# Kernel optimization log

Hardware: AMD Instinct MI355X
Metric: run time of the kernel (lower is better)

## Reference

```python
import jax, jax.numpy as jnp
import numpy as np

N_NODES = 50000
N_EDGES = 800000
D_IN = 256
D_OUT = 128


def setup_inputs() -> dict:
    key = jax.random.key(0)
    k1, k2, k3 = jax.random.split(key, 3)
    x = jax.random.normal(k1, (N_NODES, D_IN), dtype=jnp.float32)
    edge_index = jax.random.randint(k2, (2, N_EDGES), 0, N_NODES, dtype=jnp.int64)
    W = jax.random.normal(k3, (D_IN, D_OUT), dtype=jnp.float32) / np.sqrt(D_IN)
    b = jnp.zeros((D_OUT,), dtype=jnp.float32)
    prelu_a = jnp.full((D_OUT,), 0.25, dtype=jnp.float32)  # PyTorch PReLU default init
    return {"x": x, "edge_index": edge_index, "W": W, "b": b, "prelu_a": prelu_a}


def reference(x, edge_index, W, b, prelu_a):
    N = x.shape[0]
    # GCNConv default: add self-loops, symmetric deg^{-1/2} normalization
    self_loops = jnp.arange(N, dtype=edge_index.dtype)
    src = jnp.concatenate([edge_index[0], self_loops])  # message source j
    dst = jnp.concatenate([edge_index[1], self_loops])  # aggregation target i
    deg = jax.ops.segment_sum(jnp.ones_like(dst, dtype=x.dtype), dst, num_segments=N)
    dinv = jnp.where(deg > 0, jax.lax.rsqrt(deg), 0.0)
    norm = dinv[src] * dinv[dst]  # [E+N]
    h = x @ W  # [N, D_OUT] linear transform before aggregation
    msg = h[src] * norm[:, None]  # gather + scale
    out = jax.ops.segment_sum(msg, dst, num_segments=N) + b  # scatter-add + bias
    # per-channel PReLU
    return jnp.where(out > 0, out, prelu_a * out)
```

## Files before the change

### kernel.cpp

```cpp
#include <hip/hip_runtime.h>

#define N_NODES 50000
#define N_EDGES 800000
#define D_IN    256
#define D_OUT   128
#define ELL_S   64
#define GEMM_BLKS ((N_NODES + 127) / 128)
#define BKT_BLKS  ((N_EDGES + 255) / 256)
#define CNT_PAD   50176

typedef __attribute__((ext_vector_type(8))) short short8;
typedef __attribute__((ext_vector_type(4))) float floatx4;

__device__ __forceinline__ unsigned short f2bf(float f) {
    unsigned int u = __float_as_uint(f);
    unsigned int r = (u + 0x7fffu + ((u >> 16) & 1u)) >> 16;
    return (unsigned short)r;
}
__device__ __forceinline__ unsigned int pack2(float a, float b) {
    return (unsigned int)f2bf(a) | ((unsigned int)f2bf(b) << 16);
}
__device__ __forceinline__ float bfl(unsigned int u) { return __uint_as_float(u << 16); }
__device__ __forceinline__ float bfh(unsigned int u) { return __uint_as_float(u & 0xffff0000u); }

__device__ __forceinline__ int load_idx(const void* ei, int i, int is64) {
    if (is64) return (int)((const long long*)ei)[i];
    return ((const int*)ei)[i];
}

__global__ __launch_bounds__(256) void prep_kernel(const unsigned int* __restrict__ e,
                                                   int* __restrict__ is64,
                                                   const float* __restrict__ W,
                                                   unsigned short* __restrict__ bf,
                                                   int* __restrict__ cnt) {
    int bid = blockIdx.x;
    int tid = threadIdx.x;
    if (bid == 0) {
        __shared__ int found32;
        if (tid == 0) found32 = 0;
        __syncthreads();
        for (int i = tid; i < 2048; i += 256)
            if (e[2 * i + 1] != 0u) found32 = 1;
        __syncthreads();
        if (tid == 0) *is64 = (found32 ? 0 : 1);
    } else if (bid <= 16) {
        int g = (bid - 1) * 256 + tid;
        int lane = g & 63;
        int kc   = (g >> 6) & 7;
        int ct   = g >> 9;
        int n  = ct * 16 + (lane & 15);
        int kb = kc * 32 + ((lane >> 4) & 3) * 8;
        unsigned int p[4];
#pragma unroll
        for (int jj = 0; jj < 4; jj++) {
            float a = W[(size_t)(kb + 2 * jj + 0) * D_OUT + n];
            float b = W[(size_t)(kb + 2 * jj + 1) * D_OUT + n];
            p[jj] = pack2(a, b);
        }
        *(uint4*)&bf[(size_t)g * 8] = make_uint4(p[0], p[1], p[2], p[3]);
    } else {
        int i0 = ((bid - 17) * 256 + tid) * 2;
        *(int2*)&cnt[i0] = make_int2(0, 0);
    }
}

__global__ __launch_bounds__(256) void fused_kernel(const float* __restrict__ x,
                                                    const unsigned short* __restrict__ bf,
                                                    unsigned short* __restrict__ h,
                                                    const void* __restrict__ ei,
                                                    const int* __restrict__ is64p,
                                                    int* __restrict__ cnt,
                                                    int* __restrict__ bucket) {
    __shared__ unsigned short As[128][40];
    int tid = threadIdx.x;

    if (blockIdx.x >= GEMM_BLKS) {
        int e = (blockIdx.x - GEMM_BLKS) * 256 + tid;
        if (e < N_EDGES) {
            int is64 = *is64p;
            int s = load_idx(ei, e, is64);
            int d = load_idx(ei, N_EDGES + e, is64);
            int pos = atomicAdd(&cnt[d], 1);
            if (pos < ELL_S) bucket[d * ELL_S + pos] = s;
        }
        return;
    }

    int row0 = blockIdx.x * 128;
    int w    = tid >> 6;
    int lane = tid & 63;
    int quad = lane >> 4;
    int l15  = lane & 15;

    floatx4 acc[2][8];
#pragma unroll
    for (int i = 0; i < 2; i++)
#pragma unroll
        for (int j = 0; j < 8; j++) acc[i][j] = (floatx4){0.f, 0.f, 0.f, 0.f};

    int srow  = tid >> 1;
    int shalf = (tid & 1) * 16;
    const float* xrow = x + (size_t)(row0 + srow) * D_IN;
    bool svalid = (row0 + srow) < N_NODES;

    for (int k0 = 0; k0 < D_IN; k0 += 32) {
        uint4 p0 = make_uint4(0, 0, 0, 0), p1 = make_uint4(0, 0, 0, 0);
        if (svalid) {
            const float* src = xrow + k0 + shalf;
            float4 f0 = *(const float4*)(src + 0);
            float4 f1 = *(const float4*)(src + 4);
            float4 f2 = *(const float4*)(src + 8);
            float4 f3 = *(const float4*)(src + 12);
            p0 = make_uint4(pack2(f0.x, f0.y), pack2(f0.z, f0.w),
                            pack2(f1.x, f1.y), pack2(f1.z, f1.w));
            p1 = make_uint4(pack2(f2.x, f2.y), pack2(f2.z, f2.w),
                            pack2(f3.x, f3.y), pack2(f3.z, f3.w));
        }
        __syncthreads();
        *(uint4*)&As[srow][shalf + 0] = p0;
        *(uint4*)&As[srow][shalf + 8] = p1;
        __syncthreads();

        short8 a0 = *(const short8*)&As[w * 32 + l15][quad * 8];
        short8 a1 = *(const short8*)&As[w * 32 + 16 + l15][quad * 8];
        int kc = k0 >> 5;
#pragma unroll
        for (int ct = 0; ct < 8; ct++) {
            short8 b = *(const short8*)&bf[(size_t)(((ct * 8 + kc) * 64 + lane)) * 8];
            acc[0][ct] = __builtin_amdgcn_mfma_f32_16x16x32_bf16(a0, b, acc[0][ct], 0, 0, 0);
            acc[1][ct] = __builtin_amdgcn_mfma_f32_16x16x32_bf16(a1, b, acc[1][ct], 0, 0, 0);
        }
    }

#pragma unroll
    for (int rt = 0; rt < 2; rt++) {
        int grow0 = row0 + w * 32 + rt * 16 + quad * 4;
#pragma unroll
        for (int r = 0; r < 4; r++) {
            int grow = grow0 + r;
            if (grow < N_NODES) {
#pragma unroll
                for (int ct = 0; ct < 8; ct++) {
                    h[(size_t)grow * D_OUT + ct * 16 + l15] = f2bf(acc[rt][ct][r]);
                }
            }
        }
    }
}

__global__ __launch_bounds__(256) void gather_kernel(
    const unsigned short* __restrict__ h, const int* __restrict__ cnt,
    const int* __restrict__ bucket, const float* __restrict__ bias,
    const float* __restrict__ pa, float* __restrict__ out) {
    int wave = (int)((blockIdx.x * blockDim.x + threadIdx.x) >> 6);
    int lane = threadIdx.x & 63;
    if (wave >= N_NODES) return;
    int d = wave;
    int nraw = cnt[d];
    int n = nraw < ELL_S ? nraw : ELL_S;
    float di = rsqrtf((float)(nraw + 1));
    int c = lane * 2;
    const unsigned short* hrow = h + c;
    unsigned int ud = *(const unsigned int*)&hrow[(size_t)d * D_OUT];
    float sl = di * di;
    float ax = bfl(ud) * sl, ay = bfh(ud) * sl;

    int   s_l = 0;
    float w_l = 0.f;
    if (lane < n) {
        s_l = bucket[d * ELL_S + lane];
        w_l = rsqrtf((float)(cnt[s_l] + 1)) * di;
    }
    int k = 0;
    for (; k + 4 <= n; k += 4) {
        int s0 = __shfl(s_l, k + 0), s1 = __shfl(s_l, k + 1);
        int s2 = __shfl(s_l, k + 2), s3 = __shfl(s_l, k + 3);
        float w0 = __shfl(w_l, k + 0), w1 = __shfl(w_l, k + 1);
        float w2 = __shfl(w_l, k + 2), w3 = __shfl(w_l, k + 3);
        unsigned int u0 = *(const unsigned int*)&hrow[(size_t)s0 * D_OUT];
        unsigned int u1 = *(const unsigned int*)&hrow[(size_t)s1 * D_OUT];
        unsigned int u2 = *(const unsigned int*)&hrow[(size_t)s2 * D_OUT];
        unsigned int u3 = *(const unsigned int*)&hrow[(size_t)s3 * D_OUT];
        ax += bfl(u0) * w0; ay += bfh(u0) * w0;
        ax += bfl(u1) * w1; ay += bfh(u1) * w1;
        ax += bfl(u2) * w2; ay += bfh(u2) * w2;
        ax += bfl(u3) * w3; ay += bfh(u3) * w3;
    }
    for (; k < n; k++) {
        int s = __shfl(s_l, k);
        float wn = __shfl(w_l, k);
        unsigned int u = *(const unsigned int*)&hrow[(size_t)s * D_OUT];
        ax += bfl(u) * wn; ay += bfh(u) * wn;
    }
    float2 bb = *(const float2*)&bias[c];
    float2 aa = *(const float2*)&pa[c];
    float ox = ax + bb.x, oy = ay + bb.y;
    ox = ox > 0.f ? ox : aa.x * ox;
    oy = oy > 0.f ? oy : aa.y * oy;
    *(float2*)&out[(size_t)d * D_OUT + c] = make_float2(ox, oy);
}

extern "C" void kernel_launch(void* const* d_in, const int* in_sizes, int n_in,
                              void* d_out, int out_size, void* d_ws, size_t ws_size,
                              hipStream_t stream) {
    const float* x  = (const float*)d_in[0];
    const void*  ei = d_in[1];
    const float* W  = (const float*)d_in[2];
    const float* b  = (const float*)d_in[3];
    const float* pa = (const float*)d_in[4];
    float* out = (float*)d_out;

    char* w = (char*)d_ws;
    int*   is64   = (int*)w;    w += 256;
    int*   cnt    = (int*)w;    w += CNT_PAD * 4;
    unsigned short* bfrag = (unsigned short*)w; w += 8 * 8 * 64 * 8 * 2;
    int*   bucket = (int*)w;    w += (size_t)N_NODES * ELL_S * 4;
    unsigned short* h = (unsigned short*)w; w += (size_t)N_NODES * D_OUT * 2;

    prep_kernel<<<1 + 16 + 98, 256, 0, stream>>>((const unsigned int*)ei, is64, W, bfrag, cnt);
    fused_kernel<<<GEMM_BLKS + BKT_BLKS, 256, 0, stream>>>(x, bfrag, h, ei, is64, cnt, bucket);
    gather_kernel<<<(N_NODES * 64 + 255) / 256, 256, 0, stream>>>(h, cnt, bucket, b, pa, out);
}
```

Measured before the change: 169.8 us.

## Process four nodes per wave in gather and batch four edges per bucketing thread

The gather kernel now assigns each 16-lane group of a wave to its own destination node, with every lane loading 8 bf16 channels through 16-byte vector loads. The neighbor loop runs to the wave-wide maximum degree and uses shuffles within each group. This cuts wave count and gives wider memory transactions, at the cost of divergence when degrees differ inside a wave. The bucketing blocks also handle four edges per thread and issue their loads and atomics in batches to expose more memory-level parallelism.

Result: slower. 177.9 us (+4.8%).

```diff
diff --git a/kernel.cpp b/kernel.cpp
--- a/kernel.cpp
+++ b/kernel.cpp
@@ -6,7 +6,7 @@
 #define D_OUT   128
 #define ELL_S   64
 #define GEMM_BLKS ((N_NODES + 127) / 128)
-#define BKT_BLKS  ((N_EDGES + 255) / 256)
+#define BKT_BLKS  ((N_EDGES + 1023) / 1024)
 #define CNT_PAD   50176
 
 typedef __attribute__((ext_vector_type(8))) short short8;
@@ -75,14 +75,33 @@
     int tid = threadIdx.x;
 
     if (blockIdx.x >= GEMM_BLKS) {
-        int e = (blockIdx.x - GEMM_BLKS) * 256 + tid;
-        if (e < N_EDGES) {
-            int is64 = *is64p;
-            int s = load_idx(ei, e, is64);
-            int d = load_idx(ei, N_EDGES + e, is64);
-            int pos = atomicAdd(&cnt[d], 1);
-            if (pos < ELL_S) bucket[d * ELL_S + pos] = s;
-        }
+        int base = (blockIdx.x - GEMM_BLKS) * 1024 + tid;
+        int is64 = *is64p;
+        int sv[4], dv[4];
+        if (is64) {
+            const long long* p = (const long long*)ei;
+#pragma unroll
+            for (int i = 0; i < 4; i++) {
+                int e = base + i * 256;
+                if (e < N_EDGES) { sv[i] = (int)p[e]; dv[i] = (int)p[N_EDGES + e]; }
+                else { sv[i] = 0; dv[i] = -1; }
+            }
+        } else {
+            const int* p = (const int*)ei;
+#pragma unroll
+            for (int i = 0; i < 4; i++) {
+                int e = base + i * 256;
+                if (e < N_EDGES) { sv[i] = p[e]; dv[i] = p[N_EDGES + e]; }
+                else { sv[i] = 0; dv[i] = -1; }
+            }
+        }
+        int pos[4] = {ELL_S, ELL_S, ELL_S, ELL_S};
+#pragma unroll
+        for (int i = 0; i < 4; i++)
+            if (dv[i] >= 0) pos[i] = atomicAdd(&cnt[dv[i]], 1);
+#pragma unroll
+        for (int i = 0; i < 4; i++)
+            if (dv[i] >= 0 && pos[i] < ELL_S) bucket[dv[i] * ELL_S + pos[i]] = sv[i];
         return;
     }
 
@@ -148,56 +167,88 @@
     }
 }
 
+#define GACC(U, F)                                      \
+    a0 += bfl(U.x) * (F); a1 += bfh(U.x) * (F);         \
+    a2 += bfl(U.y) * (F); a3 += bfh(U.y) * (F);         \
+    a4 += bfl(U.z) * (F); a5 += bfh(U.z) * (F);         \
+    a6 += bfl(U.w) * (F); a7 += bfh(U.w) * (F);
+
+#define GBODY(SS, WW, KB)                                                         \
+    {                                                                             \
+        int lim = wave_max - (KB);                                                \
+        if (lim > 16) lim = 16;                                                   \
+        for (int k = 0; k < lim; k += 4) {                                        \
+            int   s0 = __shfl((SS), gk + k + 0), s1 = __shfl((SS), gk + k + 1);   \
+            int   s2 = __shfl((SS), gk + k + 2), s3 = __shfl((SS), gk + k + 3);   \
+            float f0 = __shfl((WW), gk + k + 0), f1 = __shfl((WW), gk + k + 1);   \
+            float f2 = __shfl((WW), gk + k + 2), f3 = __shfl((WW), gk + k + 3);   \
+            uint4 u0 = *(const uint4*)(h + (size_t)s0 * D_OUT + co);              \
+            uint4 u1 = *(const uint4*)(h + (size_t)s1 * D_OUT + co);              \
+            uint4 u2 = *(const uint4*)(h + (size_t)s2 * D_OUT + co);              \
+            uint4 u3 = *(const uint4*)(h + (size_t)s3 * D_OUT + co);              \
+            GACC(u0, f0); GACC(u1, f1); GACC(u2, f2); GACC(u3, f3);               \
+        }                                                                         \
+    }
+
 __global__ __launch_bounds__(256) void gather_kernel(
     const unsigned short* __restrict__ h, const int* __restrict__ cnt,
     const int* __restrict__ bucket, const float* __restrict__ bias,
     const float* __restrict__ pa, float* __restrict__ out) {
     int wave = (int)((blockIdx.x * blockDim.x + threadIdx.x) >> 6);
     int lane = threadIdx.x & 63;
-    if (wave >= N_NODES) return;
-    int d = wave;
+    int g  = lane >> 4;
+    int l  = lane & 15;
+    int gk = g << 4;
+    int d  = wave * 4 + g;
+
     int nraw = cnt[d];
     int n = nraw < ELL_S ? nraw : ELL_S;
     float di = rsqrtf((float)(nraw + 1));
-    int c = lane * 2;
-    const unsigned short* hrow = h + c;
-    unsigned int ud = *(const unsigned int*)&hrow[(size_t)d * D_OUT];
+
+    int co = l * 8;
+
+    uint4 us = *(const uint4*)(h + (size_t)d * D_OUT + co);
     float sl = di * di;
-    float ax = bfl(ud) * sl, ay = bfh(ud) * sl;
-
-    int   s_l = 0;
-    float w_l = 0.f;
-    if (lane < n) {
-        s_l = bucket[d * ELL_S + lane];
-        w_l = rsqrtf((float)(cnt[s_l] + 1)) * di;
-    }
-    int k = 0;
-    for (; k + 4 <= n; k += 4) {
-        int s0 = __shfl(s_l, k + 0), s1 = __shfl(s_l, k + 1);
-        int s2 = __shfl(s_l, k + 2), s3 = __shfl(s_l, k + 3);
-        float w0 = __shfl(w_l, k + 0), w1 = __shfl(w_l, k + 1);
-        float w2 = __shfl(w_l, k + 2), w3 = __shfl(w_l, k + 3);
-        unsigned int u0 = *(const unsigned int*)&hrow[(size_t)s0 * D_OUT];
-        unsigned int u1 = *(const unsigned int*)&hrow[(size_t)s1 * D_OUT];
-        unsigned int u2 = *(const unsigned int*)&hrow[(size_t)s2 * D_OUT];
-        unsigned int u3 = *(const unsigned int*)&hrow[(size_t)s3 * D_OUT];
-        ax += bfl(u0) * w0; ay += bfh(u0) * w0;
-        ax += bfl(u1) * w1; ay += bfh(u1) * w1;
-        ax += bfl(u2) * w2; ay += bfh(u2) * w2;
-        ax += bfl(u3) * w3; ay += bfh(u3) * w3;
-    }
-    for (; k < n; k++) {
-        int s = __shfl(s_l, k);
-        float wn = __shfl(w_l, k);
-        unsigned int u = *(const unsigned int*)&hrow[(size_t)s * D_OUT];
-        ax += bfl(u) * wn; ay += bfh(u) * wn;
-    }
-    float2 bb = *(const float2*)&bias[c];
-    float2 aa = *(const float2*)&pa[c];
-    float ox = ax + bb.x, oy = ay + bb.y;
-    ox = ox > 0.f ? ox : aa.x * ox;
-    oy = oy > 0.f ? oy : aa.y * oy;
-    *(float2*)&out[(size_t)d * D_OUT + c] = make_float2(ox, oy);
+    float a0 = bfl(us.x) * sl, a1 = bfh(us.x) * sl;
+    float a2 = bfl(us.y) * sl, a3 = bfh(us.y) * sl;
+    float a4 = bfl(us.z) * sl, a5 = bfh(us.z) * sl;
+    float a6 = bfl(us.w) * sl, a7 = bfh(us.w) * sl;
+
+    int db = d * ELL_S;
+    int   s0v = 0,   s1v = 0,   s2v = 0,   s3v = 0;
+    float w0v = 0.f, w1v = 0.f, w2v = 0.f, w3v = 0.f;
+    if (l      < n) { s0v = bucket[db + l];      w0v = rsqrtf((float)(cnt[s0v] + 1)) * di; }
+    if (l + 16 < n) { s1v = bucket[db + l + 16]; w1v = rsqrtf((float)(cnt[s1v] + 1)) * di; }
+    if (l + 32 < n) { s2v = bucket[db + l + 32]; w2v = rsqrtf((float)(cnt[s2v] + 1)) * di; }
+    if (l + 48 < n) { s3v = bucket[db + l + 48]; w3v = rsqrtf((float)(cnt[s3v] + 1)) * di; }
+
+    int wave_max = n;
+    { int t = __shfl_xor(wave_max, 16); wave_max = t > wave_max ? t : wave_max; }
+    { int t = __shfl_xor(wave_max, 32); wave_max = t > wave_max ? t : wave_max; }
+
+    if (wave_max > 0)  GBODY(s0v, w0v, 0)
+    if (wave_max > 16) GBODY(s1v, w1v, 16)
+    if (wave_max > 32) GBODY(s2v, w2v, 32)
+    if (wave_max > 48) GBODY(s3v, w3v, 48)
+
+    int c = l * 8;
+    float4 b0 = *(const float4*)&bias[c];
+    float4 b1 = *(const float4*)&bias[c + 4];
+    float4 p0 = *(const float4*)&pa[c];
+    float4 p1 = *(const float4*)&pa[c + 4];
+    float4 o0, o1;
+    o0.x = a0 + b0.x; o0.y = a1 + b0.y; o0.z = a2 + b0.z; o0.w = a3 + b0.w;
+    o1.x = a4 + b1.x; o1.y = a5 + b1.y; o1.z = a6 + b1.z; o1.w = a7 + b1.w;
+    o0.x = o0.x > 0.f ? o0.x : p0.x * o0.x;
+    o0.y = o0.y > 0.f ? o0.y : p0.y * o0.y;
+    o0.z = o0.z > 0.f ? o0.z : p0.z * o0.z;
+    o0.w = o0.w > 0.f ? o0.w : p0.w * o0.w;
+    o1.x = o1.x > 0.f ? o1.x : p1.x * o1.x;
+    o1.y = o1.y > 0.f ? o1.y : p1.y * o1.y;
+    o1.z = o1.z > 0.f ? o1.z : p1.z * o1.z;
+    o1.w = o1.w > 0.f ? o1.w : p1.w * o1.w;
+    *(float4*)&out[(size_t)d * D_OUT + c]     = o0;
+    *(float4*)&out[(size_t)d * D_OUT + c + 4] = o1;
 }
 
 extern "C" void kernel_launch(void* const* d_in, const int* in_sizes, int n_in,
@@ -219,5 +270,5 @@
 
     prep_kernel<<<1 + 16 + 98, 256, 0, stream>>>((const unsigned int*)ei, is64, W, bfrag, cnt);
     fused_kernel<<<GEMM_BLKS + BKT_BLKS, 256, 0, stream>>>(x, bfrag, h, ei, is64, cnt, bucket);
-    gather_kernel<<<(N_NODES * 64 + 255) / 256, 256, 0, stream>>>(h, cnt, bucket, b, pa, out);
-}
+    gather_kernel<<<(N_NODES / 4 * 64 + 255) / 256, 256, 0, stream>>>(h, cnt, bucket, b, pa, out);
+}
```
